# Kernel optimization log

Measured on AMD Instinct MI355X. Metric: run time of the kernel, lower is better.

## Reference

```python
import jax, jax.numpy as jnp
import numpy as np


def setup_inputs() -> dict:
    key = jax.random.key(0)
    kx, ks = jax.random.split(key)
    B, N, D = 2048, 65536, 64
    X = jax.random.normal(kx, (B, D), dtype=jnp.float32)
    svs = jax.random.normal(ks, (N, D), dtype=jnp.float32)
    # scale ~ 1 / mean pairwise squared distance; for iid N(0,1) data E[d^2] = 2D
    scale = jnp.asarray(1.0 / (2.0 * D), dtype=jnp.float32)
    return {"X": X, "svs": svs, "scale": scale}


def reference(X, svs, scale):
    N, D = svs.shape
    x2 = jnp.sum(X * X, axis=-1, keepdims=True)            # [B, 1]
    y2 = jnp.sum(svs * svs, axis=-1)                       # [N]
    d2 = x2 + y2[None, :] - 2.0 * jnp.einsum('bd,nd->bn', X, svs)  # [B, N]
    log_p = (jax.scipy.special.logsumexp(-scale * d2, axis=-1)
             - jnp.log(jnp.asarray(N, dtype=X.dtype))
             + (D / 2) * jnp.log(scale / jnp.pi))
    return log_p
```

## Files before the change

### kernel.cpp

```cpp
#include <hip/hip_runtime.h>
#include <hip/hip_bf16.h>

typedef __attribute__((ext_vector_type(8))) short short8;
typedef __attribute__((ext_vector_type(4))) float f32x4;

#define LOG2E 1.4426950408889634f
#define PI_F 3.14159265358979323846f
#define NTOT 65536
#define BTOT 2048
#define DIM 64
#define SPLITS 64
#define NITER 8
#define NTILES 512

#define OFF_SVSBF 0u
#define OFF_XBF   8388608u
#define OFF_EB2   8650752u
#define OFF_A2    8912896u
#define OFF_PART  8921088u
#define WS_NEEDED 9969664u

__device__ __forceinline__ unsigned short f2bf(float f) {
    union { __hip_bfloat16 h; unsigned short u; } c;
    c.h = __float2bfloat16(f);
    return c.u;
}

__device__ __forceinline__ int swz(int row, int kbyte) {
    return row * 128 + (kbyte ^ ((row & 7) << 4));
}

__global__ __launch_bounds__(256) void kde_prep(
    const float* __restrict__ X, const float* __restrict__ svs,
    const float* __restrict__ scale_p, unsigned short* __restrict__ svs_bf,
    unsigned short* __restrict__ x_bf, float* __restrict__ eb2,
    float* __restrict__ a2nat) {
    const float scale = scale_p[0];
    const int tid = threadIdx.x;
    const int blk = blockIdx.x;
    if (blk < NTILES) {
#pragma unroll
        for (int i = 0; i < 4; ++i) {
            int g = i * 256 + tid;
            int row = g >> 3, grp = g & 7;
            const float* src = svs + ((size_t)blk * 128 + row) * DIM + grp * 8;
            float4 v0 = *(const float4*)src;
            float4 v1 = *(const float4*)(src + 4);
            float ss = v0.x * v0.x + v0.y * v0.y + v0.z * v0.z + v0.w * v0.w +
                       v1.x * v1.x + v1.y * v1.y + v1.z * v1.z + v1.w * v1.w;
            short8 o;
            o[0] = f2bf(v0.x); o[1] = f2bf(v0.y); o[2] = f2bf(v0.z); o[3] = f2bf(v0.w);
            o[4] = f2bf(v1.x); o[5] = f2bf(v1.y); o[6] = f2bf(v1.z); o[7] = f2bf(v1.w);
            int dgrp = grp ^ (row & 7);
            *(short8*)(svs_bf + (size_t)blk * 8192 + row * 64 + dgrp * 8) = o;
            ss += __shfl_xor(ss, 1, 64);
            ss += __shfl_xor(ss, 2, 64);
            ss += __shfl_xor(ss, 4, 64);
            if (grp == 0)
                eb2[blk * 128 + row] = __builtin_amdgcn_exp2f(-scale * LOG2E * ss);
        }
    } else {
        const int t16 = blk - NTILES;
        const float C1 = 2.0f * scale * LOG2E;
#pragma unroll
        for (int i = 0; i < 4; ++i) {
            int g = i * 256 + tid;
            int row = g >> 3, grp = g & 7;
            const float* src = X + ((size_t)t16 * 128 + row) * DIM + grp * 8;
            float4 v0 = *(const float4*)src;
            float4 v1 = *(const float4*)(src + 4);
            float ss = v0.x * v0.x + v0.y * v0.y + v0.z * v0.z + v0.w * v0.w +
                       v1.x * v1.x + v1.y * v1.y + v1.z * v1.z + v1.w * v1.w;
            short8 o;
            o[0] = f2bf(v0.x * C1); o[1] = f2bf(v0.y * C1);
            o[2] = f2bf(v0.z * C1); o[3] = f2bf(v0.w * C1);
            o[4] = f2bf(v1.x * C1); o[5] = f2bf(v1.y * C1);
            o[6] = f2bf(v1.z * C1); o[7] = f2bf(v1.w * C1);
            *(short8*)(x_bf + ((size_t)t16 * 128 + row) * 64 + grp * 8) = o;
            ss += __shfl_xor(ss, 1, 64);
            ss += __shfl_xor(ss, 2, 64);
            ss += __shfl_xor(ss, 4, 64);
            if (grp == 0) a2nat[t16 * 128 + row] = -scale * ss;
        }
    }
}

__global__ __launch_bounds__(256) void kde_main4(
    const unsigned short* __restrict__ svs_bf,
    const unsigned short* __restrict__ x_bf, const float* __restrict__ eb2,
    float* __restrict__ partials) {
    __shared__ __align__(16) unsigned char ldsB[2][16384];
    __shared__ __align__(16) float ldseb2[1024];

    const int tid = threadIdx.x, lane = tid & 63, wave = tid >> 6;
    const int bid = blockIdx.x;
    const int xcd = bid & 7, j = bid >> 3;
    const int nsplit = ((j & 7) << 3) | xcd;
    const int mtile = j >> 3;
    const int rowbase = mtile * 128;
    const int wm = wave >> 1, wn = wave & 1;
    const int col = lane & 15, krow = lane >> 4;

    short8 afrag[4][2];
#pragma unroll
    for (int mf = 0; mf < 4; ++mf) {
        int arow = rowbase + wm * 64 + mf * 16 + col;
#pragma unroll
        for (int kf = 0; kf < 2; ++kf)
            afrag[mf][kf] =
                *(const short8*)(x_bf + (size_t)arow * 64 + krow * 8 + kf * 32);
    }
    asm volatile("s_waitcnt vmcnt(0)" ::: "memory");

    {
        const float* gb = eb2 + nsplit * 1024 + wave * 256 + lane * 4;
        __builtin_amdgcn_global_load_lds(
            (const __attribute__((address_space(1))) void*)gb,
            (__attribute__((address_space(3))) void*)&ldseb2[wave * 256], 16, 0, 0);
    }
    const unsigned char* gsv =
        (const unsigned char*)svs_bf + (size_t)nsplit * NITER * 16384;
#define ISSUE_TILE(t_, buf_)                                                      \
    do {                                                                          \
        const unsigned char* gt =                                                 \
            gsv + (size_t)(t_)*16384 + (size_t)wave * 4096 + lane * 16;           \
        for (int ii = 0; ii < 4; ++ii)                                            \
            __builtin_amdgcn_global_load_lds(                                     \
                (const __attribute__((address_space(1))) void*)(gt + ii * 1024),  \
                (__attribute__((address_space(3))) void*)&ldsB[buf_][(wave * 4 + ii) * 1024], \
                16, 0, 0);                                                        \
    } while (0)
    ISSUE_TILE(0, 0);
    ISSUE_TILE(1, 1);

    const f32x4 zacc = {0.f, 0.f, 0.f, 0.f};
    float s[4][4];
#pragma unroll
    for (int mf = 0; mf < 4; ++mf)
#pragma unroll
        for (int q = 0; q < 4; ++q) s[mf][q] = 0.f;

#pragma unroll
    for (int it = 0; it < NITER; ++it) {
        if (it < NITER - 1)
            asm volatile("s_waitcnt vmcnt(4)" ::: "memory");
        else
            asm volatile("s_waitcnt vmcnt(0)" ::: "memory");
        asm volatile("s_barrier" ::: "memory");
        const unsigned char* buf = ldsB[it & 1];
#pragma unroll
        for (int nf = 0; nf < 4; ++nf) {
            int brow = wn * 64 + nf * 16 + col;
            int kb = krow * 16;
            short8 bb0 = *(const short8*)(buf + swz(brow, kb));
            short8 bb1 = *(const short8*)(buf + swz(brow, kb + 64));
            float eb2l = ldseb2[it * 128 + wn * 64 + nf * 16 + col];
#pragma unroll
            for (int mf = 0; mf < 4; ++mf) {
                f32x4 acc = __builtin_amdgcn_mfma_f32_16x16x32_bf16(
                    afrag[mf][0], bb0, zacc, 0, 0, 0);
                acc = __builtin_amdgcn_mfma_f32_16x16x32_bf16(afrag[mf][1], bb1,
                                                              acc, 0, 0, 0);
                s[mf][0] = __builtin_fmaf(__builtin_amdgcn_exp2f(acc[0]), eb2l, s[mf][0]);
                s[mf][1] = __builtin_fmaf(__builtin_amdgcn_exp2f(acc[1]), eb2l, s[mf][1]);
                s[mf][2] = __builtin_fmaf(__builtin_amdgcn_exp2f(acc[2]), eb2l, s[mf][2]);
                s[mf][3] = __builtin_fmaf(__builtin_amdgcn_exp2f(acc[3]), eb2l, s[mf][3]);
            }
        }
        asm volatile("s_barrier" ::: "memory");
        if (it + 2 < NITER) ISSUE_TILE(it + 2, it & 1);
    }
#undef ISSUE_TILE

#pragma unroll
    for (int mask = 1; mask < 16; mask <<= 1)
#pragma unroll
        for (int mf = 0; mf < 4; ++mf)
#pragma unroll
            for (int q = 0; q < 4; ++q)
                s[mf][q] += __shfl_xor(s[mf][q], mask, 64);

    if (col == 0) {
#pragma unroll
        for (int mf = 0; mf < 4; ++mf)
#pragma unroll
            for (int q = 0; q < 4; ++q) {
                int row = rowbase + wm * 64 + mf * 16 + krow * 4 + q;
                partials[(size_t)(nsplit * 2 + wn) * BTOT + row] = s[mf][q];
            }
    }
}

__global__ void kde_final4(const float* __restrict__ partials,
                           const float* __restrict__ a2nat,
                           const float* __restrict__ scale_p,
                           float* __restrict__ out) {
    int b = blockIdx.x * 256 + threadIdx.x;
    if (b >= BTOT) return;
    float total = 0.f;
    for (int sidx = 0; sidx < SPLITS * 2; ++sidx)
        total += partials[(size_t)sidx * BTOT + b];
    out[b] = logf(total) + a2nat[b] - logf((float)NTOT) +
             32.0f * logf(scale_p[0] / PI_F);
}

__global__ void fb_rownorm(const float* __restrict__ in,
                           const float* __restrict__ scale_p,
                           float* __restrict__ out, int nrows) {
    int t = blockIdx.x * 256 + threadIdx.x;
    int row = t >> 4;
    if (row >= nrows) return;
    int c4 = t & 15;
    float4 v = *(const float4*)&in[(size_t)row * 64 + c4 * 4];
    float ss = v.x * v.x + v.y * v.y + v.z * v.z + v.w * v.w;
    ss += __shfl_xor(ss, 1, 64);
    ss += __shfl_xor(ss, 2, 64);
    ss += __shfl_xor(ss, 4, 64);
    ss += __shfl_xor(ss, 8, 64);
    if (c4 == 0) out[row] = -scale_p[0] * LOG2E * ss;
}

__global__ __launch_bounds__(256) void fb_main(
    const float* __restrict__ X, const float* __restrict__ svs,
    const float* __restrict__ scale_p, const float* __restrict__ a2,
    const float* __restrict__ b2, float* __restrict__ partials) {
    __shared__ __align__(16) unsigned char ldsA[128 * 128];
    __shared__ __align__(16) unsigned char ldsBf[128 * 128];
    const int tid = threadIdx.x, lane = tid & 63, wave = tid >> 6;
    const int rowbase = blockIdx.x * 128, nbase = blockIdx.y * 512;
    const float C1 = 2.0f * scale_p[0] * LOG2E;
    {
        int r16 = tid >> 4, c4 = tid & 15;
        for (int p = 0; p < 8; ++p) {
            int row = p * 16 + r16;
            float4 v = *(const float4*)&X[(size_t)(rowbase + row) * 64 + c4 * 4];
            uint2 pk;
            pk.x = (unsigned)f2bf(v.x) | ((unsigned)f2bf(v.y) << 16);
            pk.y = (unsigned)f2bf(v.z) | ((unsigned)f2bf(v.w) << 16);
            *(uint2*)(ldsA + swz(row, c4 * 8)) = pk;
        }
    }
    __syncthreads();
    short8 afrag[2][2];
    {
        int arow = wave * 32 + (lane & 15);
        int kb = (lane >> 4) * 16;
        for (int mf = 0; mf < 2; ++mf)
            for (int kf = 0; kf < 2; ++kf)
                afrag[mf][kf] = *(const short8*)(ldsA + swz(arow + mf * 16, kb + kf * 64));
    }
    float a2l[2][4];
    for (int mf = 0; mf < 2; ++mf)
        for (int q = 0; q < 4; ++q)
            a2l[mf][q] = a2[rowbase + wave * 32 + mf * 16 + (lane >> 4) * 4 + q];
    float s[2][4] = {{0.f, 0.f, 0.f, 0.f}, {0.f, 0.f, 0.f, 0.f}};
    for (int itq = 0; itq < 4; ++itq) {
        int nb0 = nbase + itq * 128;
        __syncthreads();
        {
            int r16 = tid >> 4, c4 = tid & 15;
            for (int p = 0; p < 8; ++p) {
                int row = p * 16 + r16;
                float4 v = *(const float4*)&svs[(size_t)(nb0 + row) * 64 + c4 * 4];
                uint2 pk;
                pk.x = (unsigned)f2bf(v.x) | ((unsigned)f2bf(v.y) << 16);
                pk.y = (unsigned)f2bf(v.z) | ((unsigned)f2bf(v.w) << 16);
                *(uint2*)(ldsBf + swz(row, c4 * 8)) = pk;
            }
        }
        float b2l[8];
        for (int nf = 0; nf < 8; ++nf)
            b2l[nf] = b2[nb0 + nf * 16 + (lane & 15)];
        __syncthreads();
        for (int nf = 0; nf < 8; ++nf) {
            int brow = nf * 16 + (lane & 15);
            int kb = (lane >> 4) * 16;
            short8 b0 = *(const short8*)(ldsBf + swz(brow, kb));
            short8 b1 = *(const short8*)(ldsBf + swz(brow, kb + 64));
            for (int mf = 0; mf < 2; ++mf) {
                f32x4 acc = {0.f, 0.f, 0.f, 0.f};
                acc = __builtin_amdgcn_mfma_f32_16x16x32_bf16(afrag[mf][0], b0, acc, 0, 0, 0);
                acc = __builtin_amdgcn_mfma_f32_16x16x32_bf16(afrag[mf][1], b1, acc, 0, 0, 0);
                for (int q = 0; q < 4; ++q) {
                    float e = __builtin_fmaf(C1, acc[q], a2l[mf][q]) + b2l[nf];
                    s[mf][q] += __builtin_amdgcn_exp2f(e);
                }
            }
        }
    }
    for (int mask = 1; mask < 16; mask <<= 1)
        for (int mf = 0; mf < 2; ++mf)
            for (int q = 0; q < 4; ++q)
                s[mf][q] += __shfl_xor(s[mf][q], mask, 64);
    if ((lane & 15) == 0) {
        for (int mf = 0; mf < 2; ++mf)
            for (int q = 0; q < 4; ++q) {
                int row = rowbase + wave * 32 + mf * 16 + (lane >> 4) * 4 + q;
                partials[(size_t)blockIdx.y * BTOT + row] = s[mf][q];
            }
    }
}

__global__ void fb_final(const float* __restrict__ partials,
                         const float* __restrict__ scale_p,
                         float* __restrict__ out) {
    int b = blockIdx.x * 256 + threadIdx.x;
    if (b >= BTOT) return;
    float total = 0.f;
    for (int sidx = 0; sidx < 128; ++sidx)
        total += partials[(size_t)sidx * BTOT + b];
    out[b] = logf(total) - logf((float)NTOT) + 32.0f * logf(scale_p[0] / PI_F);
}

extern "C" void kernel_launch(void* const* d_in, const int* in_sizes, int n_in,
                              void* d_out, int out_size, void* d_ws,
                              size_t ws_size, hipStream_t stream) {
    const float* X = (const float*)d_in[0];
    const float* svs = (const float*)d_in[1];
    const float* scale_p = (const float*)d_in[2];
    unsigned char* ws = (unsigned char*)d_ws;

    if (ws_size >= WS_NEEDED) {
        unsigned short* svs_bf = (unsigned short*)(ws + OFF_SVSBF);
        unsigned short* x_bf = (unsigned short*)(ws + OFF_XBF);
        float* eb2 = (float*)(ws + OFF_EB2);
        float* a2nat = (float*)(ws + OFF_A2);
        float* partials = (float*)(ws + OFF_PART);
        kde_prep<<<NTILES + 16, 256, 0, stream>>>(X, svs, scale_p, svs_bf, x_bf,
                                                  eb2, a2nat);
        kde_main4<<<BTOT / 128 * SPLITS, 256, 0, stream>>>(svs_bf, x_bf, eb2,
                                                           partials);
        kde_final4<<<BTOT / 256, 256, 0, stream>>>(partials, a2nat, scale_p,
                                                   (float*)d_out);
    } else {
        float* wsf = (float*)d_ws;
        float* b2 = wsf;
        float* a2 = wsf + NTOT;
        float* partials = wsf + NTOT + BTOT;
        fb_rownorm<<<(NTOT * 16) / 256, 256, 0, stream>>>(svs, scale_p, b2, NTOT);
        fb_rownorm<<<(BTOT * 16) / 256, 256, 0, stream>>>(X, scale_p, a2, BTOT);
        dim3 grid(BTOT / 128, 128);
        fb_main<<<grid, 256, 0, stream>>>(X, svs, scale_p, a2, b2, partials);
        fb_final<<<BTOT / 256, 256, 0, stream>>>(partials, scale_p, (float*)d_out);
    }
}
```

Baseline: 52.53 us.

## Drop LDS staging; stream B fragments from global with register prefetch

The main kernel no longer stages svs tiles in double-buffered LDS with barriers. Each wave now owns a 64-row strip of X and reads its B fragments and eb2 values straight from global (cache) memory, prefetching the next fragment into registers. The grid is reshaped to 128 N-splits with 4 independent waves per block, and the swizzled prep layout is removed. This removes LDS traffic and barrier synchronisation, at the cost of redundant global/L2 reads of svs across the waves and a longer per-wave serial loop.

```diff
diff --git a/kernel.cpp b/kernel.cpp
--- a/kernel.cpp
+++ b/kernel.cpp
@@ -9,8 +9,7 @@
 #define NTOT 65536
 #define BTOT 2048
 #define DIM 64
-#define SPLITS 64
-#define NITER 8
+#define NSPL 128
 #define NTILES 512
 
 #define OFF_SVSBF 0u
@@ -24,10 +23,6 @@
     union { __hip_bfloat16 h; unsigned short u; } c;
     c.h = __float2bfloat16(f);
     return c.u;
-}
-
-__device__ __forceinline__ int swz(int row, int kbyte) {
-    return row * 128 + (kbyte ^ ((row & 7) << 4));
 }
 
 __global__ __launch_bounds__(256) void kde_prep(
@@ -51,8 +46,7 @@
             short8 o;
             o[0] = f2bf(v0.x); o[1] = f2bf(v0.y); o[2] = f2bf(v0.z); o[3] = f2bf(v0.w);
             o[4] = f2bf(v1.x); o[5] = f2bf(v1.y); o[6] = f2bf(v1.z); o[7] = f2bf(v1.w);
-            int dgrp = grp ^ (row & 7);
-            *(short8*)(svs_bf + (size_t)blk * 8192 + row * 64 + dgrp * 8) = o;
+            *(short8*)(svs_bf + (size_t)blk * 8192 + row * 64 + grp * 8) = o;
             ss += __shfl_xor(ss, 1, 64);
             ss += __shfl_xor(ss, 2, 64);
             ss += __shfl_xor(ss, 4, 64);
@@ -85,53 +79,31 @@
     }
 }
 
-__global__ __launch_bounds__(256) void kde_main4(
+__global__ __launch_bounds__(256) void kde_main5(
     const unsigned short* __restrict__ svs_bf,
     const unsigned short* __restrict__ x_bf, const float* __restrict__ eb2,
     float* __restrict__ partials) {
-    __shared__ __align__(16) unsigned char ldsB[2][16384];
-    __shared__ __align__(16) float ldseb2[1024];
-
     const int tid = threadIdx.x, lane = tid & 63, wave = tid >> 6;
     const int bid = blockIdx.x;
     const int xcd = bid & 7, j = bid >> 3;
-    const int nsplit = ((j & 7) << 3) | xcd;
-    const int mtile = j >> 3;
-    const int rowbase = mtile * 128;
-    const int wm = wave >> 1, wn = wave & 1;
+    const int nsplit = ((j & 15) << 3) | xcd;
+    const int mgroup = j >> 4;
+    const int mstrip = mgroup * 4 + wave;
+    const int rowbase = mstrip * 64;
     const int col = lane & 15, krow = lane >> 4;
 
     short8 afrag[4][2];
 #pragma unroll
     for (int mf = 0; mf < 4; ++mf) {
-        int arow = rowbase + wm * 64 + mf * 16 + col;
+        const unsigned short* ap =
+            x_bf + (size_t)(rowbase + mf * 16 + col) * 64 + krow * 8;
 #pragma unroll
         for (int kf = 0; kf < 2; ++kf)
-            afrag[mf][kf] =
-                *(const short8*)(x_bf + (size_t)arow * 64 + krow * 8 + kf * 32);
-    }
-    asm volatile("s_waitcnt vmcnt(0)" ::: "memory");
-
-    {
-        const float* gb = eb2 + nsplit * 1024 + wave * 256 + lane * 4;
-        __builtin_amdgcn_global_load_lds(
-            (const __attribute__((address_space(1))) void*)gb,
-            (__attribute__((address_space(3))) void*)&ldseb2[wave * 256], 16, 0, 0);
-    }
-    const unsigned char* gsv =
-        (const unsigned char*)svs_bf + (size_t)nsplit * NITER * 16384;
-#define ISSUE_TILE(t_, buf_)                                                      \
-    do {                                                                          \
-        const unsigned char* gt =                                                 \
-            gsv + (size_t)(t_)*16384 + (size_t)wave * 4096 + lane * 16;           \
-        for (int ii = 0; ii < 4; ++ii)                                            \
-            __builtin_amdgcn_global_load_lds(                                     \
-                (const __attribute__((address_space(1))) void*)(gt + ii * 1024),  \
-                (__attribute__((address_space(3))) void*)&ldsB[buf_][(wave * 4 + ii) * 1024], \
-                16, 0, 0);                                                        \
-    } while (0)
-    ISSUE_TILE(0, 0);
-    ISSUE_TILE(1, 1);
+            afrag[mf][kf] = *(const short8*)(ap + kf * 32);
+    }
+
+    const unsigned short* bbase = svs_bf + (size_t)nsplit * 512 * 64;
+    const float* ebase = eb2 + nsplit * 512;
 
     const f32x4 zacc = {0.f, 0.f, 0.f, 0.f};
     float s[4][4];
@@ -140,37 +112,33 @@
 #pragma unroll
         for (int q = 0; q < 4; ++q) s[mf][q] = 0.f;
 
-#pragma unroll
-    for (int it = 0; it < NITER; ++it) {
-        if (it < NITER - 1)
-            asm volatile("s_waitcnt vmcnt(4)" ::: "memory");
-        else
-            asm volatile("s_waitcnt vmcnt(0)" ::: "memory");
-        asm volatile("s_barrier" ::: "memory");
-        const unsigned char* buf = ldsB[it & 1];
-#pragma unroll
-        for (int nf = 0; nf < 4; ++nf) {
-            int brow = wn * 64 + nf * 16 + col;
-            int kb = krow * 16;
-            short8 bb0 = *(const short8*)(buf + swz(brow, kb));
-            short8 bb1 = *(const short8*)(buf + swz(brow, kb + 64));
-            float eb2l = ldseb2[it * 128 + wn * 64 + nf * 16 + col];
-#pragma unroll
-            for (int mf = 0; mf < 4; ++mf) {
-                f32x4 acc = __builtin_amdgcn_mfma_f32_16x16x32_bf16(
-                    afrag[mf][0], bb0, zacc, 0, 0, 0);
-                acc = __builtin_amdgcn_mfma_f32_16x16x32_bf16(afrag[mf][1], bb1,
-                                                              acc, 0, 0, 0);
-                s[mf][0] = __builtin_fmaf(__builtin_amdgcn_exp2f(acc[0]), eb2l, s[mf][0]);
-                s[mf][1] = __builtin_fmaf(__builtin_amdgcn_exp2f(acc[1]), eb2l, s[mf][1]);
-                s[mf][2] = __builtin_fmaf(__builtin_amdgcn_exp2f(acc[2]), eb2l, s[mf][2]);
-                s[mf][3] = __builtin_fmaf(__builtin_amdgcn_exp2f(acc[3]), eb2l, s[mf][3]);
-            }
-        }
-        asm volatile("s_barrier" ::: "memory");
-        if (it + 2 < NITER) ISSUE_TILE(it + 2, it & 1);
-    }
-#undef ISSUE_TILE
+    const unsigned short* bp0 = bbase + (size_t)col * 64 + krow * 8;
+    short8 nb0 = *(const short8*)bp0;
+    short8 nb1 = *(const short8*)(bp0 + 32);
+    float ne = ebase[col];
+
+#pragma unroll 4
+    for (int step = 0; step < 32; ++step) {
+        short8 cb0 = nb0, cb1 = nb1;
+        float ce = ne;
+        int nxt = (step + 1) & 31;
+        const unsigned short* bp =
+            bbase + (size_t)(nxt * 16 + col) * 64 + krow * 8;
+        nb0 = *(const short8*)bp;
+        nb1 = *(const short8*)(bp + 32);
+        ne = ebase[nxt * 16 + col];
+#pragma unroll
+        for (int mf = 0; mf < 4; ++mf) {
+            f32x4 acc = __builtin_amdgcn_mfma_f32_16x16x32_bf16(afrag[mf][0],
+                                                                cb0, zacc, 0, 0, 0);
+            acc = __builtin_amdgcn_mfma_f32_16x16x32_bf16(afrag[mf][1], cb1,
+                                                          acc, 0, 0, 0);
+            s[mf][0] = __builtin_fmaf(__builtin_amdgcn_exp2f(acc[0]), ce, s[mf][0]);
+            s[mf][1] = __builtin_fmaf(__builtin_amdgcn_exp2f(acc[1]), ce, s[mf][1]);
+            s[mf][2] = __builtin_fmaf(__builtin_amdgcn_exp2f(acc[2]), ce, s[mf][2]);
+            s[mf][3] = __builtin_fmaf(__builtin_amdgcn_exp2f(acc[3]), ce, s[mf][3]);
+        }
+    }
 
 #pragma unroll
     for (int mask = 1; mask < 16; mask <<= 1)
@@ -185,23 +153,27 @@
         for (int mf = 0; mf < 4; ++mf)
 #pragma unroll
             for (int q = 0; q < 4; ++q) {
-                int row = rowbase + wm * 64 + mf * 16 + krow * 4 + q;
-                partials[(size_t)(nsplit * 2 + wn) * BTOT + row] = s[mf][q];
+                int row = rowbase + mf * 16 + krow * 4 + q;
+                partials[(size_t)nsplit * BTOT + row] = s[mf][q];
             }
     }
 }
 
-__global__ void kde_final4(const float* __restrict__ partials,
+__global__ void kde_final5(const float* __restrict__ partials,
                            const float* __restrict__ a2nat,
                            const float* __restrict__ scale_p,
                            float* __restrict__ out) {
     int b = blockIdx.x * 256 + threadIdx.x;
     if (b >= BTOT) return;
     float total = 0.f;
-    for (int sidx = 0; sidx < SPLITS * 2; ++sidx)
+    for (int sidx = 0; sidx < NSPL; ++sidx)
         total += partials[(size_t)sidx * BTOT + b];
     out[b] = logf(total) + a2nat[b] - logf((float)NTOT) +
              32.0f * logf(scale_p[0] / PI_F);
+}
+
+__device__ __forceinline__ int swz(int row, int kbyte) {
+    return row * 128 + (kbyte ^ ((row & 7) << 4));
 }
 
 __global__ void fb_rownorm(const float* __restrict__ in,
@@ -328,9 +300,8 @@
         float* partials = (float*)(ws + OFF_PART);
         kde_prep<<<NTILES + 16, 256, 0, stream>>>(X, svs, scale_p, svs_bf, x_bf,
                                                   eb2, a2nat);
-        kde_main4<<<BTOT / 128 * SPLITS, 256, 0, stream>>>(svs_bf, x_bf, eb2,
-                                                           partials);
-        kde_final4<<<BTOT / 256, 256, 0, stream>>>(partials, a2nat, scale_p,
+        kde_main5<<<1024, 256, 0, stream>>>(svs_bf, x_bf, eb2, partials);
+        kde_final5<<<BTOT / 256, 256, 0, stream>>>(partials, a2nat, scale_p,
                                                    (float*)d_out);
     } else {
         float* wsf = (float*)d_ws;
```

After: 51.30 us. -2.4%, faster.

## Split N into 128 chunks with 8-wave blocks and smaller per-wave tiles

Applied to the files above, without the earlier changes.

The main kernel now splits the support vectors into 128 chunks instead of 64 and uses 512-thread blocks of 8 waves, each wave computing a 32x32 output tile instead of 64x64. Each stage loads a 64-row bf16 tile, so LDS staging is smaller, and the grid doubles to 2048 blocks to raise occupancy and latency hiding. The cost is less register-level reuse (more LDS fragment reads per MFMA), twice as many partial sums for the final reduction to write and read, and a 4-byte LDS load for the eb2 weights.

```diff
diff --git a/kernel.cpp b/kernel.cpp
--- a/kernel.cpp
+++ b/kernel.cpp
@@ -9,7 +9,7 @@
 #define NTOT 65536
 #define BTOT 2048
 #define DIM 64
-#define SPLITS 64
+#define NSPL 128
 #define NITER 8
 #define NTILES 512
 
@@ -18,16 +18,12 @@
 #define OFF_EB2   8650752u
 #define OFF_A2    8912896u
 #define OFF_PART  8921088u
-#define WS_NEEDED 9969664u
+#define WS_NEEDED 11018240u
 
 __device__ __forceinline__ unsigned short f2bf(float f) {
     union { __hip_bfloat16 h; unsigned short u; } c;
     c.h = __float2bfloat16(f);
     return c.u;
-}
-
-__device__ __forceinline__ int swz(int row, int kbyte) {
-    return row * 128 + (kbyte ^ ((row & 7) << 4));
 }
 
 __global__ __launch_bounds__(256) void kde_prep(
@@ -85,78 +81,73 @@
     }
 }
 
-__global__ __launch_bounds__(256) void kde_main4(
+__global__ __launch_bounds__(512) void kde_main9(
     const unsigned short* __restrict__ svs_bf,
     const unsigned short* __restrict__ x_bf, const float* __restrict__ eb2,
     float* __restrict__ partials) {
-    __shared__ __align__(16) unsigned char ldsB[2][16384];
-    __shared__ __align__(16) float ldseb2[1024];
+    __shared__ __align__(16) unsigned char ldsB[2][8192];
+    __shared__ __align__(16) float ebl[512];
 
     const int tid = threadIdx.x, lane = tid & 63, wave = tid >> 6;
     const int bid = blockIdx.x;
     const int xcd = bid & 7, j = bid >> 3;
-    const int nsplit = ((j & 7) << 3) | xcd;
-    const int mtile = j >> 3;
-    const int rowbase = mtile * 128;
+    const int nsplit = ((j & 15) << 3) | xcd;
+    const int mtile = j >> 4;
     const int wm = wave >> 1, wn = wave & 1;
+    const int rowbase = mtile * 128 + wm * 32;
     const int col = lane & 15, krow = lane >> 4;
-
-    short8 afrag[4][2];
-#pragma unroll
-    for (int mf = 0; mf < 4; ++mf) {
-        int arow = rowbase + wm * 64 + mf * 16 + col;
+    const int off0 = (krow ^ (col & 7)) << 4;
+    const int off1 = ((krow + 4) ^ (col & 7)) << 4;
+
+    short8 afrag[2][2];
+#pragma unroll
+    for (int mf = 0; mf < 2; ++mf) {
+        const unsigned short* ap =
+            x_bf + (size_t)(rowbase + mf * 16 + col) * 64 + krow * 8;
 #pragma unroll
         for (int kf = 0; kf < 2; ++kf)
-            afrag[mf][kf] =
-                *(const short8*)(x_bf + (size_t)arow * 64 + krow * 8 + kf * 32);
+            afrag[mf][kf] = *(const short8*)(ap + kf * 32);
     }
     asm volatile("s_waitcnt vmcnt(0)" ::: "memory");
 
     {
-        const float* gb = eb2 + nsplit * 1024 + wave * 256 + lane * 4;
+        const float* gb = eb2 + nsplit * 512 + wave * 64 + lane;
         __builtin_amdgcn_global_load_lds(
             (const __attribute__((address_space(1))) void*)gb,
-            (__attribute__((address_space(3))) void*)&ldseb2[wave * 256], 16, 0, 0);
+            (__attribute__((address_space(3))) void*)&ebl[wave * 64], 4, 0, 0);
     }
     const unsigned char* gsv =
-        (const unsigned char*)svs_bf + (size_t)nsplit * NITER * 16384;
-#define ISSUE_TILE(t_, buf_)                                                      \
+        (const unsigned char*)svs_bf + (size_t)nsplit * 65536;
+#define STAGE(t_, buf_)                                                           \
     do {                                                                          \
-        const unsigned char* gt =                                                 \
-            gsv + (size_t)(t_)*16384 + (size_t)wave * 4096 + lane * 16;           \
-        for (int ii = 0; ii < 4; ++ii)                                            \
-            __builtin_amdgcn_global_load_lds(                                     \
-                (const __attribute__((address_space(1))) void*)(gt + ii * 1024),  \
-                (__attribute__((address_space(3))) void*)&ldsB[buf_][(wave * 4 + ii) * 1024], \
-                16, 0, 0);                                                        \
+        const unsigned char* gt_ = gsv + (size_t)(t_)*8192 + wave * 1024 + lane * 16; \
+        __builtin_amdgcn_global_load_lds(                                         \
+            (const __attribute__((address_space(1))) void*)gt_,                   \
+            (__attribute__((address_space(3))) void*)&ldsB[buf_][wave * 1024],    \
+            16, 0, 0);                                                            \
     } while (0)
-    ISSUE_TILE(0, 0);
-    ISSUE_TILE(1, 1);
+    STAGE(0, 0);
+    STAGE(1, 1);
 
     const f32x4 zacc = {0.f, 0.f, 0.f, 0.f};
-    float s[4][4];
-#pragma unroll
-    for (int mf = 0; mf < 4; ++mf)
-#pragma unroll
-        for (int q = 0; q < 4; ++q) s[mf][q] = 0.f;
+    float s[2][4] = {{0.f, 0.f, 0.f, 0.f}, {0.f, 0.f, 0.f, 0.f}};
 
 #pragma unroll
     for (int it = 0; it < NITER; ++it) {
         if (it < NITER - 1)
-            asm volatile("s_waitcnt vmcnt(4)" ::: "memory");
+            asm volatile("s_waitcnt vmcnt(1)" ::: "memory");
         else
             asm volatile("s_waitcnt vmcnt(0)" ::: "memory");
         asm volatile("s_barrier" ::: "memory");
         const unsigned char* buf = ldsB[it & 1];
 #pragma unroll
-        for (int nf = 0; nf < 4; ++nf) {
-            int brow = wn * 64 + nf * 16 + col;
-            int kb = krow * 16;
-            short8 bb0 = *(const short8*)(buf + swz(brow, kb));
-            short8 bb1 = *(const short8*)(buf + swz(brow, kb + 64));
-            float eb2l = ldseb2[it * 128 + wn * 64 + nf * 16 + col];
-#pragma unroll
-            for (int mf = 0; mf < 4; ++mf) {
+        for (int nf = 0; nf < 2; ++nf) {
+            const int brow = wn * 32 + nf * 16 + col;
+            short8 bb0 = *(const short8*)(buf + brow * 128 + off0);
+            short8 bb1 = *(const short8*)(buf + brow * 128 + off1);
+            float eb2l = ebl[it * 64 + wn * 32 + nf * 16 + col];
+#pragma unroll
+            for (int mf = 0; mf < 2; ++mf) {
                 f32x4 acc = __builtin_amdgcn_mfma_f32_16x16x32_bf16(
                     afrag[mf][0], bb0, zacc, 0, 0, 0);
                 acc = __builtin_amdgcn_mfma_f32_16x16x32_bf16(afrag[mf][1], bb1,
@@ -168,40 +159,44 @@
             }
         }
         asm volatile("s_barrier" ::: "memory");
-        if (it + 2 < NITER) ISSUE_TILE(it + 2, it & 1);
-    }
-#undef ISSUE_TILE
+        if (it + 2 < NITER) STAGE(it + 2, it & 1);
+    }
+#undef STAGE
 
 #pragma unroll
     for (int mask = 1; mask < 16; mask <<= 1)
 #pragma unroll
-        for (int mf = 0; mf < 4; ++mf)
+        for (int mf = 0; mf < 2; ++mf)
 #pragma unroll
             for (int q = 0; q < 4; ++q)
                 s[mf][q] += __shfl_xor(s[mf][q], mask, 64);
 
     if (col == 0) {
 #pragma unroll
-        for (int mf = 0; mf < 4; ++mf)
+        for (int mf = 0; mf < 2; ++mf)
 #pragma unroll
             for (int q = 0; q < 4; ++q) {
-                int row = rowbase + wm * 64 + mf * 16 + krow * 4 + q;
+                int row = rowbase + mf * 16 + krow * 4 + q;
                 partials[(size_t)(nsplit * 2 + wn) * BTOT + row] = s[mf][q];
             }
     }
 }
 
-__global__ void kde_final4(const float* __restrict__ partials,
+__global__ void kde_final9(const float* __restrict__ partials,
                            const float* __restrict__ a2nat,
                            const float* __restrict__ scale_p,
                            float* __restrict__ out) {
     int b = blockIdx.x * 256 + threadIdx.x;
     if (b >= BTOT) return;
     float total = 0.f;
-    for (int sidx = 0; sidx < SPLITS * 2; ++sidx)
+    for (int sidx = 0; sidx < NSPL * 2; ++sidx)
         total += partials[(size_t)sidx * BTOT + b];
     out[b] = logf(total) + a2nat[b] - logf((float)NTOT) +
              32.0f * logf(scale_p[0] / PI_F);
+}
+
+__device__ __forceinline__ int swz(int row, int kbyte) {
+    return row * 128 + (kbyte ^ ((row & 7) << 4));
 }
 
 __global__ void fb_rownorm(const float* __restrict__ in,
@@ -328,9 +323,8 @@
         float* partials = (float*)(ws + OFF_PART);
         kde_prep<<<NTILES + 16, 256, 0, stream>>>(X, svs, scale_p, svs_bf, x_bf,
                                                   eb2, a2nat);
-        kde_main4<<<BTOT / 128 * SPLITS, 256, 0, stream>>>(svs_bf, x_bf, eb2,
-                                                           partials);
-        kde_final4<<<BTOT / 256, 256, 0, stream>>>(partials, a2nat, scale_p,
+        kde_main9<<<2048, 512, 0, stream>>>(svs_bf, x_bf, eb2, partials);
+        kde_final9<<<BTOT / 256, 256, 0, stream>>>(partials, a2nat, scale_p,
                                                    (float*)d_out);
     } else {
         float* wsf = (float*)d_ws;
```

New measurement: 48.16 us. 8.3% less time.
